# Kernel tuning notes

Measured on AMD Instinct MI355X. Metric: run time of the kernel, lower is better.

## Reference

```python
import jax, jax.numpy as jnp
import numpy as np

B, S, DIM = 2, 2048, 1024
N_HEAD, HEAD_DIM = 16, 64


def setup_inputs() -> dict:
    key = jax.random.key(0)
    k1, k2, k3, k4 = jax.random.split(key, 4)
    x = jax.random.normal(k1, (B, S, DIM), dtype=jnp.float32)
    # rotary table: cos/sin pairs, shape [S, head_dim//2, 2]
    half = HEAD_DIM // 2
    inv_freq = 1.0 / (10000.0 ** (jnp.arange(0, half, dtype=jnp.float32) / half))
    t = jnp.arange(S, dtype=jnp.float32)
    ang = t[:, None] * inv_freq[None, :]
    freqs_cis = jnp.stack([jnp.cos(ang), jnp.sin(ang)], axis=-1)  # [S, half, 2]
    # causal boolean mask [1,1,S,S] (True = attend)
    mask = jnp.tril(jnp.ones((S, S), dtype=bool))[None, None]
    wqkv = jax.random.normal(k2, (3 * DIM, DIM), dtype=jnp.float32) * (DIM ** -0.5)
    wo = jax.random.normal(k3, (DIM, DIM), dtype=jnp.float32) * (DIM ** -0.5)
    return {"x": x, "freqs_cis": freqs_cis, "mask": mask, "wqkv": wqkv, "wo": wo}


def apply_rotary_emb(x, freqs_cis):
    # x: [B, S, H, D]; freqs_cis: [S, D//2, 2]
    xs = x.reshape(*x.shape[:-1], -1, 2)  # [B,S,H,D//2,2]
    fc = freqs_cis[None, :, None, :, :]  # [1,S,1,D//2,2]
    xr, xi = xs[..., 0], xs[..., 1]
    cr, ci = fc[..., 0], fc[..., 1]
    out = jnp.stack([xr * cr - xi * ci, xi * cr + xr * ci], axis=-1)
    return out.reshape(x.shape)


def reference(x, freqs_cis, mask, wqkv, wo):
    bsz, seqlen, _ = x.shape
    qkv = jnp.einsum('bsd,ed->bse', x, wqkv)  # [B,S,3*dim]
    q, k, v = jnp.split(qkv, 3, axis=-1)
    q = q.reshape(bsz, seqlen, N_HEAD, HEAD_DIM)
    k = k.reshape(bsz, seqlen, N_HEAD, HEAD_DIM)
    v = v.reshape(bsz, seqlen, N_HEAD, HEAD_DIM)
    q = apply_rotary_emb(q, freqs_cis)
    k = apply_rotary_emb(k, freqs_cis)
    scale = HEAD_DIM ** -0.5
    scores = jnp.einsum('bqhd,bkhd->bhqk', q, k) * scale  # [B,H,S,S]
    scores = jnp.where(mask, scores, jnp.finfo(scores.dtype).min)
    attn = jax.nn.softmax(scores, axis=-1)
    y = jnp.einsum('bhqk,bkhd->bqhd', attn, v).reshape(bsz, seqlen, N_HEAD * HEAD_DIM)
    return jnp.einsum('bse,de->bsd', y, wo)
```

## Files before the change

### kernel.cpp

```cpp
#include <hip/hip_runtime.h>
#include <hip/hip_bf16.h>
#include <stdint.h>


typedef __attribute__((ext_vector_type(8))) __bf16 bf16x8;
typedef __attribute__((ext_vector_type(4))) float f32x4;
typedef __attribute__((ext_vector_type(16))) float f32x16;

union B8 { uint4 u; bf16x8 v; unsigned short us[8]; };

static __device__ __forceinline__ float bf2f(unsigned short u) {
  union { unsigned int ui; float f; } x; x.ui = ((unsigned int)u) << 16; return x.f;
}
static __device__ __forceinline__ unsigned short f2bf(float f) {
  union { float f; unsigned int ui; } x; x.f = f;
  unsigned int r = x.ui + 0x7fffu + ((x.ui >> 16) & 1u);
  return (unsigned short)(r >> 16);
}
static __device__ __forceinline__ f32x4 mfma16(bf16x8 a, bf16x8 b, f32x4 c) {
  return __builtin_amdgcn_mfma_f32_16x16x32_bf16(a, b, c, 0, 0, 0);
}
static __device__ __forceinline__ f32x16 mfma32(bf16x8 a, bf16x8 b, f32x16 c) {
  return __builtin_amdgcn_mfma_f32_32x32x16_bf16(a, b, c, 0, 0, 0);
}
#define AS1 __attribute__((address_space(1)))
#define AS3 __attribute__((address_space(3)))
static __device__ __forceinline__ void gload_lds16(const void* g, void* l) {
  __builtin_amdgcn_global_load_lds((const AS1 unsigned int*)g,
                                   (AS3 unsigned int*)l, 16, 0, 0);
}

__global__ __launch_bounds__(256) void cvt_all_kernel(
    const float* __restrict__ x, const float* __restrict__ wqkv,
    const float* __restrict__ wo,
    unsigned short* __restrict__ xb, unsigned short* __restrict__ wqkvb,
    unsigned short* __restrict__ wob) {
  int i = blockIdx.x * 256 + threadIdx.x;
  const float* src; unsigned short* dst; int off;
  if (i < 1048576)       { src = x;    dst = xb;    off = i; }
  else if (i < 1835008)  { src = wqkv; dst = wqkvb; off = i - 1048576; }
  else                   { src = wo;   dst = wob;   off = i - 1835008; }
  float4 f = ((const float4*)src)[off];
  ushort4 u;
  u.x = f2bf(f.x); u.y = f2bf(f.y); u.z = f2bf(f.z); u.w = f2bf(f.w);
  ((ushort4*)dst)[off] = u;
}

__global__ __launch_bounds__(256) void qkv_rope_kernel(
    const unsigned short* __restrict__ xb,
    const unsigned short* __restrict__ wqkvb,
    const float* __restrict__ freqs,
    unsigned short* __restrict__ Q,
    unsigned short* __restrict__ K,
    unsigned short* __restrict__ Vt)
{
  __shared__ __align__(16) unsigned short As[128 * 64];
  __shared__ __align__(16) unsigned short Bs[128 * 64];
  const int t = threadIdx.x;
  const int lane = t & 63, wv = t >> 6;
  const int l31 = lane & 31, lh = lane >> 5;
  const int wm = wv >> 1, wn = wv & 1;
  const int tm = blockIdx.x & 31, tn = blockIdx.x >> 5;
  const int m0 = tm * 128, n0 = tn * 128;

  f32x16 acc[2][2] = {};

  for (int k0 = 0; k0 < 1024; k0 += 64) {
    for (int r = 0; r < 4; ++r) {
      int cid = t + 256 * r;
      int row = cid >> 3, jc = cid & 7;
      int sc = jc ^ (row & 7);
      gload_lds16(xb    + (size_t)(m0 + row) * 1024 + k0 + sc * 8, (char*)As + cid * 16);
      gload_lds16(wqkvb + (size_t)(n0 + row) * 1024 + k0 + sc * 8, (char*)Bs + cid * 16);
    }
    __syncthreads();
    for (int kst = 0; kst < 4; ++kst) {
      const int g = kst * 2 + lh;
      bf16x8 a[2], b[2];
      for (int s2 = 0; s2 < 2; ++s2) {
        int ra = wm * 64 + s2 * 32 + l31;
        a[s2] = *(const bf16x8*)((const char*)As + ra * 128 + (g ^ (ra & 7)) * 16);
        int rb = wn * 64 + s2 * 32 + l31;
        b[s2] = *(const bf16x8*)((const char*)Bs + rb * 128 + (g ^ (rb & 7)) * 16);
      }
      for (int sm = 0; sm < 2; ++sm)
        for (int sn = 0; sn < 2; ++sn)
          acc[sm][sn] = mfma32(a[sm], b[sn], acc[sm][sn]);
    }
    __syncthreads();
  }

  for (int sm = 0; sm < 2; ++sm) {
    for (int sn = 0; sn < 2; ++sn) {
      const int e = n0 + wn * 64 + sn * 32 + l31;
      const int seg = e >> 10;
      const int eh = e & 1023;
      const int h = eh >> 6, d = eh & 63;
      for (int r = 0; r < 16; ++r) {
        const int m = m0 + wm * 64 + sm * 32 + (r & 3) + 8 * (r >> 2) + 4 * lh;
        const int b_ = m >> 11, s_ = m & 2047;
        float v = acc[sm][sn][r];
        if (seg == 2) {
          Vt[((size_t)(b_ * 16 + h) * 64 + d) * 2048 + s_] = f2bf(v);
        } else {
          float partner = __shfl_xor(v, 1, 64);
          float cr = freqs[s_ * 64 + (d & ~1)];
          float ci = freqs[s_ * 64 + (d | 1)];
          float outv = (d & 1) ? (v * cr + partner * ci) : (v * cr - partner * ci);
          unsigned short* dst = (seg == 0) ? Q : K;
          dst[((size_t)(b_ * 16 + h) * 2048 + s_) * 64 + d] = f2bf(outv);
        }
      }
    }
  }
}

struct QState {
  bf16x8 qf0, qf1;
  f32x4 o[4];
  float lp[4];
};

static __device__ __forceinline__ void load_q(QState& st,
    const unsigned short* Qb, int q0, int c, int quad) {
  st.qf0 = *(const bf16x8*)(Qb + (q0 + c) * 64 + quad * 8);
  st.qf1 = *(const bf16x8*)(Qb + (q0 + c) * 64 + 32 + quad * 8);
}

static __device__ __forceinline__ void attn_chunk(
    QState& st, const char* Ks, const char* Vs, float* myp,
    int c, int quad, int k0, int q0, bool diag)
{
  f32x4 sfr[4];
  for (int kc = 0; kc < 4; ++kc) {
    const int key = kc * 16 + c;
    const int s0 = quad ^ (key & 7), s1 = (4 + quad) ^ (key & 7);
    f32x4 sacc = {};
    sacc = mfma16(st.qf0, *(const bf16x8*)(Ks + key * 128 + s0 * 16), sacc);
    sacc = mfma16(st.qf1, *(const bf16x8*)(Ks + key * 128 + s1 * 16), sacc);
    sfr[kc] = sacc;
  }
  for (int i = 0; i < 4; ++i) {
    const int qrow = q0 + quad * 4 + i;
    float e[4];
    for (int kc = 0; kc < 4; ++kc) {
      float arg = fmaf(sfr[kc][i], 0.18033688f, -20.19773057f);
      if (diag && (k0 + kc * 16 + c > qrow)) arg = -1e30f;
      e[kc] = exp2f(arg);
    }
    st.lp[i] += (e[0] + e[1]) + (e[2] + e[3]);
    const int prow = (quad * 4 + i) * 68;
    myp[prow + c]      = e[0];
    myp[prow + 16 + c] = e[1];
    myp[prow + 32 + c] = e[2];
    myp[prow + 48 + c] = e[3];
  }
  bf16x8 pf[2];
  for (int sH = 0; sH < 2; ++sH) {
    const float* src = myp + c * 68 + sH * 32 + quad * 8;
    float4 f0 = *(const float4*)(src);
    float4 f1 = *(const float4*)(src + 4);
    B8 p;
    p.us[0] = f2bf(f0.x); p.us[1] = f2bf(f0.y);
    p.us[2] = f2bf(f0.z); p.us[3] = f2bf(f0.w);
    p.us[4] = f2bf(f1.x); p.us[5] = f2bf(f1.y);
    p.us[6] = f2bf(f1.z); p.us[7] = f2bf(f1.w);
    pf[sH] = p.v;
  }
  for (int ct = 0; ct < 4; ++ct) {
    const int d = ct * 16 + c;
    const int s0 = quad ^ (d & 7), s1 = (4 + quad) ^ (d & 7);
    st.o[ct] = mfma16(pf[0], *(const bf16x8*)(Vs + d * 128 + s0 * 16), st.o[ct]);
    st.o[ct] = mfma16(pf[1], *(const bf16x8*)(Vs + d * 128 + s1 * 16), st.o[ct]);
  }
}

static __device__ __forceinline__ void write_state(
    QState& st, int q0, int c, int quad,
    unsigned short* Poh, float* Plh)
{
  for (int i = 0; i < 4; ++i) {
    float l = st.lp[i];
    l += __shfl_xor(l, 1, 16);
    l += __shfl_xor(l, 2, 16);
    l += __shfl_xor(l, 4, 16);
    l += __shfl_xor(l, 8, 16);
    const int s = q0 + quad * 4 + i;
    for (int ct = 0; ct < 4; ++ct)
      Poh[(size_t)s * 64 + ct * 16 + c] = f2bf(st.o[ct][i]);
    if (c == 0) Plh[s] = l;
  }
}

__global__ __launch_bounds__(256) void attn_partial_kernel(
    const unsigned short* __restrict__ Q,
    const unsigned short* __restrict__ K,
    const unsigned short* __restrict__ Vt,
    unsigned short* __restrict__ Po,
    float* __restrict__ Pl)
{
  __shared__ __align__(16) unsigned short Ks[64 * 64];
  __shared__ __align__(16) unsigned short Vs[64 * 64];
  __shared__ __align__(16) float plds[4][16 * 68];
  const int t = threadIdx.x;
  const int lane = t & 63, wv = t >> 6;
  const int c = lane & 15, quad = lane >> 4;
  const int bh = blockIdx.x & 31;
  const int rr = blockIdx.x >> 5;
  const int k8 = rr >> 1, half = rr & 1;
  const int j0 = 2 * k8, j1 = 2 * k8 + 1;
  const int qA0 = j0 * 64 + wv * 16,  qB0 = (31 - j0) * 64 + wv * 16;
  const int qA1 = j1 * 64 + wv * 16,  qB1 = (31 - j1) * 64 + wv * 16;

  const unsigned short* Qb = Q + (size_t)bh * (2048 * 64);
  const unsigned short* Kb = K + (size_t)bh * (2048 * 64);
  const unsigned short* Vb = Vt + (size_t)bh * (64 * 2048);

  QState A0 = {}, A1 = {}, B0 = {}, B1 = {};
  load_q(A0, Qb, qA0, c, quad);
  load_q(A1, Qb, qA1, c, quad);
  load_q(B0, Qb, qB0, c, quad);
  load_q(B1, Qb, qB1, c, quad);

  float* myp = plds[wv];
  const int ktmax = 31 - j0;

  for (int kt = half; kt <= ktmax; kt += 2) {
    const int k0 = kt * 64;
    __syncthreads();
    for (int r = 0; r < 2; ++r) {
      int cid = t + 256 * r;
      int row = cid >> 3, jc = cid & 7;
      int sc = jc ^ (row & 7);
      gload_lds16(Kb + (size_t)(k0 + row) * 64 + sc * 8, (char*)Ks + cid * 16);
      gload_lds16(Vb + (size_t)row * 2048 + k0 + sc * 8, (char*)Vs + cid * 16);
    }
    __syncthreads();
    attn_chunk(B0, (const char*)Ks, (const char*)Vs, myp, c, quad,
               k0, qB0, kt == 31 - j0);
    if (kt <= 31 - j1)
      attn_chunk(B1, (const char*)Ks, (const char*)Vs, myp, c, quad,
                 k0, qB1, kt == 31 - j1);
    if (kt <= j1)
      attn_chunk(A1, (const char*)Ks, (const char*)Vs, myp, c, quad,
                 k0, qA1, kt == j1);
    if (kt <= j0)
      attn_chunk(A0, (const char*)Ks, (const char*)Vs, myp, c, quad,
                 k0, qA0, kt == j0);
  }

  unsigned short* Poh = Po + (size_t)half * (32 * 2048 * 64) + (size_t)bh * (2048 * 64);
  float* Plh = Pl + (size_t)half * (32 * 2048) + bh * 2048;
  write_state(A0, qA0, c, quad, Poh, Plh);
  write_state(A1, qA1, c, quad, Poh, Plh);
  write_state(B0, qB0, c, quad, Poh, Plh);
  write_state(B1, qB1, c, quad, Poh, Plh);
}

__global__ __launch_bounds__(256) void attn_kernel(
    const unsigned short* __restrict__ Q,
    const unsigned short* __restrict__ K,
    const unsigned short* __restrict__ Vt,
    unsigned short* __restrict__ Y)
{
  __shared__ __align__(16) unsigned short Ks[64 * 64];
  __shared__ __align__(16) unsigned short Vs[64 * 64];
  __shared__ __align__(16) float plds[4][16 * 68];
  const int t = threadIdx.x;
  const int lane = t & 63, wv = t >> 6;
  const int c = lane & 15, quad = lane >> 4;
  const int j = blockIdx.x >> 5, bh = blockIdx.x & 31;
  const int b = bh >> 4, h = bh & 15;
  const int qA = j * 64 + wv * 16;
  const int qB = (31 - j) * 64 + wv * 16;

  const unsigned short* Qb = Q + (size_t)bh * (2048 * 64);
  const unsigned short* Kb = K + (size_t)bh * (2048 * 64);
  const unsigned short* Vb = Vt + (size_t)bh * (64 * 2048);

  QState A = {}, Bst = {};
  load_q(A, Qb, qA, c, quad);
  load_q(Bst, Qb, qB, c, quad);

  const int nkt = 32 - j;
  float* myp = plds[wv];

  for (int kt = 0; kt < nkt; ++kt) {
    const int k0 = kt * 64;
    __syncthreads();
    for (int r = 0; r < 2; ++r) {
      int cid = t + 256 * r;
      int row = cid >> 3, jc = cid & 7;
      int sc = jc ^ (row & 7);
      gload_lds16(Kb + (size_t)(k0 + row) * 64 + sc * 8, (char*)Ks + cid * 16);
      gload_lds16(Vb + (size_t)row * 2048 + k0 + sc * 8, (char*)Vs + cid * 16);
    }
    __syncthreads();
    attn_chunk(Bst, (const char*)Ks, (const char*)Vs, myp, c, quad,
               k0, qB, kt == 31 - j);
    if (kt <= j)
      attn_chunk(A, (const char*)Ks, (const char*)Vs, myp, c, quad,
                 k0, qA, kt == j);
  }

  for (int set = 0; set < 2; ++set) {
    QState& st = set ? Bst : A;
    const int q0 = set ? qB : qA;
    for (int i = 0; i < 4; ++i) {
      float l = st.lp[i];
      l += __shfl_xor(l, 1, 16);
      l += __shfl_xor(l, 2, 16);
      l += __shfl_xor(l, 4, 16);
      l += __shfl_xor(l, 8, 16);
      float inv = 1.0f / l;
      const int s = q0 + quad * 4 + i;
      unsigned short* dst = Y + ((size_t)(b * 2048 + s)) * 1024 + h * 64;
      for (int ct = 0; ct < 4; ++ct)
        dst[ct * 16 + c] = f2bf(st.o[ct][i] * inv);
    }
  }
}

__global__ __launch_bounds__(256) void out_proj_fused_kernel(
    const unsigned short* __restrict__ Po, const float* __restrict__ Pl,
    const unsigned short* __restrict__ wob,
    float* __restrict__ out)
{
  __shared__ __align__(16) unsigned short As[64 * 64];
  __shared__ __align__(16) unsigned short Bs[64 * 64];
  const int t = threadIdx.x;
  const int lane = t & 63, wv = t >> 6;
  const int c = lane & 15, quad = lane >> 4;
  const int wm = wv >> 1, wn = wv & 1;
  const int tm = blockIdx.x & 63, tn = blockIdx.x >> 6;
  const int m0 = tm * 64, n0 = tn * 64;

  f32x4 acc[2][2] = {};

  for (int k0 = 0; k0 < 1024; k0 += 64) {
    const int h = k0 >> 6;
    for (int r = 0; r < 2; ++r) {
      int cid = t + 256 * r;
      int row = cid >> 3, jc = cid & 7;
      int sc = jc ^ (row & 7);
      gload_lds16(wob + (size_t)(n0 + row) * 1024 + k0 + sc * 8, (char*)Bs + cid * 16);
      const int m = m0 + row, b_ = m >> 11, s = m & 2047;
      const int bh = b_ * 16 + h;
      const size_t base = (size_t)bh * (2048 * 64) + (size_t)s * 64 + sc * 8;
      B8 pa, pb, y;
      pa.u = *(const uint4*)(Po + base);
      pb.u = *(const uint4*)(Po + (size_t)(32 * 2048 * 64) + base);
      float l = Pl[bh * 2048 + s] + Pl[32 * 2048 + bh * 2048 + s];
      float inv = 1.0f / l;
      for (int k = 0; k < 8; ++k)
        y.us[k] = f2bf((bf2f(pa.us[k]) + bf2f(pb.us[k])) * inv);
      *(uint4*)((char*)As + cid * 16) = y.u;
    }
    __syncthreads();
    for (int ks = 0; ks < 2; ++ks) {
      bf16x8 a[2], b[2];
      for (int st = 0; st < 2; ++st) {
        int ra = wm * 32 + st * 16 + c;
        int sa = (ks * 4 + quad) ^ (ra & 7);
        a[st] = *(const bf16x8*)((const char*)As + ra * 128 + sa * 16);
        int rb = wn * 32 + st * 16 + c;
        int sb = (ks * 4 + quad) ^ (rb & 7);
        b[st] = *(const bf16x8*)((const char*)Bs + rb * 128 + sb * 16);
      }
      for (int sm = 0; sm < 2; ++sm)
        for (int sn = 0; sn < 2; ++sn)
          acc[sm][sn] = mfma16(a[sm], b[sn], acc[sm][sn]);
    }
    __syncthreads();
  }

  for (int sm = 0; sm < 2; ++sm)
    for (int sn = 0; sn < 2; ++sn)
      for (int i = 0; i < 4; ++i) {
        const int m = m0 + wm * 32 + sm * 16 + quad * 4 + i;
        const int e = n0 + wn * 32 + sn * 16 + c;
        out[(size_t)m * 1024 + e] = acc[sm][sn][i];
      }
}

__global__ __launch_bounds__(256) void out_proj_kernel(
    const unsigned short* __restrict__ Y,
    const unsigned short* __restrict__ wob,
    float* __restrict__ out)
{
  __shared__ __align__(16) unsigned short As[64 * 64];
  __shared__ __align__(16) unsigned short Bs[64 * 64];
  const int t = threadIdx.x;
  const int lane = t & 63, wv = t >> 6;
  const int c = lane & 15, quad = lane >> 4;
  const int wm = wv >> 1, wn = wv & 1;
  const int tm = blockIdx.x & 63, tn = blockIdx.x >> 6;
  const int m0 = tm * 64, n0 = tn * 64;

  f32x4 acc[2][2] = {};

  for (int k0 = 0; k0 < 1024; k0 += 64) {
    for (int r = 0; r < 2; ++r) {
      int cid = t + 256 * r;
      int row = cid >> 3, jc = cid & 7;
      int sc = jc ^ (row & 7);
      gload_lds16(Y   + (size_t)(m0 + row) * 1024 + k0 + sc * 8, (char*)As + cid * 16);
      gload_lds16(wob + (size_t)(n0 + row) * 1024 + k0 + sc * 8, (char*)Bs + cid * 16);
    }
    __syncthreads();
    for (int ks = 0; ks < 2; ++ks) {
      bf16x8 a[2], b[2];
      for (int st = 0; st < 2; ++st) {
        int ra = wm * 32 + st * 16 + c;
        int sa = (ks * 4 + quad) ^ (ra & 7);
        a[st] = *(const bf16x8*)((const char*)As + ra * 128 + sa * 16);
        int rb = wn * 32 + st * 16 + c;
        int sb = (ks * 4 + quad) ^ (rb & 7);
        b[st] = *(const bf16x8*)((const char*)Bs + rb * 128 + sb * 16);
      }
      for (int sm = 0; sm < 2; ++sm)
        for (int sn = 0; sn < 2; ++sn)
          acc[sm][sn] = mfma16(a[sm], b[sn], acc[sm][sn]);
    }
    __syncthreads();
  }

  for (int sm = 0; sm < 2; ++sm)
    for (int sn = 0; sn < 2; ++sn)
      for (int i = 0; i < 4; ++i) {
        const int m = m0 + wm * 32 + sm * 16 + quad * 4 + i;
        const int e = n0 + wn * 32 + sn * 16 + c;
        out[(size_t)m * 1024 + e] = acc[sm][sn][i];
      }
}

extern "C" void kernel_launch(void* const* d_in, const int* in_sizes, int n_in,
                              void* d_out, int out_size, void* d_ws, size_t ws_size,
                              hipStream_t stream) {
  const float* x     = (const float*)d_in[0];
  const float* freqs = (const float*)d_in[1];
  const float* wqkv  = (const float*)d_in[3];
  const float* wo    = (const float*)d_in[4];
  float* out = (float*)d_out;

  const size_t BHSD = (size_t)2 * 16 * 2048 * 64;
  unsigned short* Q     = (unsigned short*)d_ws;
  unsigned short* K     = Q + BHSD;
  unsigned short* Vt    = K + BHSD;
  unsigned short* Yb    = Vt + BHSD;
  unsigned short* xb    = Yb + BHSD;
  unsigned short* wqkvb = xb + 4194304;
  unsigned short* wob   = wqkvb + 3145728;
  unsigned short* Po    = wob + 1048576;
  float*          Pl    = (float*)(Po + 2 * BHSD);

  const size_t need_fast =
      (size_t)((char*)(Pl + 2 * 32 * 2048) - (char*)d_ws);

  cvt_all_kernel<<<8192, 256, 0, stream>>>(x, wqkv, wo, xb, wqkvb, wob);
  qkv_rope_kernel<<<768, 256, 0, stream>>>(xb, wqkvb, freqs, Q, K, Vt);
  if (ws_size >= need_fast) {
    attn_partial_kernel<<<512, 256, 0, stream>>>(Q, K, Vt, Po, Pl);
    out_proj_fused_kernel<<<1024, 256, 0, stream>>>(Po, Pl, wob, out);
  } else {
    attn_kernel<<<512, 256, 0, stream>>>(Q, K, Vt, Yb);
    out_proj_kernel<<<1024, 256, 0, stream>>>(Yb, wob, out);
  }
}
```

Before: 248.9 us.

## Split attention partial blocks to one q-tile pair each, doubling grid size

Each attention-partial block now handles one paired (j, 31-j) query-tile set instead of two adjacent pairs, and the grid grows from 512 to 1024 blocks. The aim is more parallelism and fewer live accumulator registers per thread, which should improve occupancy and load balance across CUs. In exchange, each K/V chunk loaded into LDS is reused by fewer query tiles, so global-to-LDS traffic roughly doubles.

```diff
diff --git a/kernel.cpp b/kernel.cpp
--- a/kernel.cpp
+++ b/kernel.cpp
@@ -175,23 +175,6 @@
   }
 }
 
-static __device__ __forceinline__ void write_state(
-    QState& st, int q0, int c, int quad,
-    unsigned short* Poh, float* Plh)
-{
-  for (int i = 0; i < 4; ++i) {
-    float l = st.lp[i];
-    l += __shfl_xor(l, 1, 16);
-    l += __shfl_xor(l, 2, 16);
-    l += __shfl_xor(l, 4, 16);
-    l += __shfl_xor(l, 8, 16);
-    const int s = q0 + quad * 4 + i;
-    for (int ct = 0; ct < 4; ++ct)
-      Poh[(size_t)s * 64 + ct * 16 + c] = f2bf(st.o[ct][i]);
-    if (c == 0) Plh[s] = l;
-  }
-}
-
 __global__ __launch_bounds__(256) void attn_partial_kernel(
     const unsigned short* __restrict__ Q,
     const unsigned short* __restrict__ K,
@@ -206,24 +189,21 @@
   const int lane = t & 63, wv = t >> 6;
   const int c = lane & 15, quad = lane >> 4;
   const int bh = blockIdx.x & 31;
-  const int rr = blockIdx.x >> 5;
-  const int k8 = rr >> 1, half = rr & 1;
-  const int j0 = 2 * k8, j1 = 2 * k8 + 1;
-  const int qA0 = j0 * 64 + wv * 16,  qB0 = (31 - j0) * 64 + wv * 16;
-  const int qA1 = j1 * 64 + wv * 16,  qB1 = (31 - j1) * 64 + wv * 16;
+  const int rest = blockIdx.x >> 5;
+  const int j = rest >> 1, half = rest & 1;
+  const int qA = j * 64 + wv * 16;
+  const int qB = (31 - j) * 64 + wv * 16;
 
   const unsigned short* Qb = Q + (size_t)bh * (2048 * 64);
   const unsigned short* Kb = K + (size_t)bh * (2048 * 64);
   const unsigned short* Vb = Vt + (size_t)bh * (64 * 2048);
 
-  QState A0 = {}, A1 = {}, B0 = {}, B1 = {};
-  load_q(A0, Qb, qA0, c, quad);
-  load_q(A1, Qb, qA1, c, quad);
-  load_q(B0, Qb, qB0, c, quad);
-  load_q(B1, Qb, qB1, c, quad);
+  QState A = {}, Bst = {};
+  load_q(A, Qb, qA, c, quad);
+  load_q(Bst, Qb, qB, c, quad);
 
   float* myp = plds[wv];
-  const int ktmax = 31 - j0;
+  const int ktmax = 31 - j;
 
   for (int kt = half; kt <= ktmax; kt += 2) {
     const int k0 = kt * 64;
@@ -236,25 +216,30 @@
       gload_lds16(Vb + (size_t)row * 2048 + k0 + sc * 8, (char*)Vs + cid * 16);
     }
     __syncthreads();
-    attn_chunk(B0, (const char*)Ks, (const char*)Vs, myp, c, quad,
-               k0, qB0, kt == 31 - j0);
-    if (kt <= 31 - j1)
-      attn_chunk(B1, (const char*)Ks, (const char*)Vs, myp, c, quad,
-                 k0, qB1, kt == 31 - j1);
-    if (kt <= j1)
-      attn_chunk(A1, (const char*)Ks, (const char*)Vs, myp, c, quad,
-                 k0, qA1, kt == j1);
-    if (kt <= j0)
-      attn_chunk(A0, (const char*)Ks, (const char*)Vs, myp, c, quad,
-                 k0, qA0, kt == j0);
+    attn_chunk(Bst, (const char*)Ks, (const char*)Vs, myp, c, quad,
+               k0, qB, kt == ktmax);
+    if (kt <= j)
+      attn_chunk(A, (const char*)Ks, (const char*)Vs, myp, c, quad,
+                 k0, qA, kt == j);
   }
 
   unsigned short* Poh = Po + (size_t)half * (32 * 2048 * 64) + (size_t)bh * (2048 * 64);
   float* Plh = Pl + (size_t)half * (32 * 2048) + bh * 2048;
-  write_state(A0, qA0, c, quad, Poh, Plh);
-  write_state(A1, qA1, c, quad, Poh, Plh);
-  write_state(B0, qB0, c, quad, Poh, Plh);
-  write_state(B1, qB1, c, quad, Poh, Plh);
+  for (int set = 0; set < 2; ++set) {
+    QState& st = set ? Bst : A;
+    const int q0 = set ? qB : qA;
+    for (int i = 0; i < 4; ++i) {
+      float l = st.lp[i];
+      l += __shfl_xor(l, 1, 16);
+      l += __shfl_xor(l, 2, 16);
+      l += __shfl_xor(l, 4, 16);
+      l += __shfl_xor(l, 8, 16);
+      const int s = q0 + quad * 4 + i;
+      for (int ct = 0; ct < 4; ++ct)
+        Poh[(size_t)s * 64 + ct * 16 + c] = f2bf(st.o[ct][i]);
+      if (c == 0) Plh[s] = l;
+    }
+  }
 }
 
 __global__ __launch_bounds__(256) void attn_kernel(
@@ -460,7 +445,7 @@
   cvt_all_kernel<<<8192, 256, 0, stream>>>(x, wqkv, wo, xb, wqkvb, wob);
   qkv_rope_kernel<<<768, 256, 0, stream>>>(xb, wqkvb, freqs, Q, K, Vt);
   if (ws_size >= need_fast) {
-    attn_partial_kernel<<<512, 256, 0, stream>>>(Q, K, Vt, Po, Pl);
+    attn_partial_kernel<<<1024, 256, 0, stream>>>(Q, K, Vt, Po, Pl);
     out_proj_fused_kernel<<<1024, 256, 0, stream>>>(Po, Pl, wob, out);
   } else {
     attn_kernel<<<512, 256, 0, stream>>>(Q, K, Vt, Yb);
```

Measured after the change: 229.0 us. 8.0% less time.
